# Kernel tuning notes

Measured on AMD Instinct MI355X. Metric: run time of the kernel, lower is better.

Reference implementation:

```python
import jax, jax.numpy as jnp
import numpy as np

DIM = 1024
H = 16
DH = DIM // H
EPS = 1e-5
NEG = -1e38


def _layernorm(x, g, b):
    m = jnp.mean(x, axis=-1, keepdims=True)
    v = jnp.mean((x - m) ** 2, axis=-1, keepdims=True)
    return (x - m) / jnp.sqrt(v + EPS) * g + b


def setup_inputs() -> dict:
    key = jax.random.key(0)
    ks = jax.random.split(key, 12)
    B, Nq, Nk = 4, 1024, 1024
    Q = jax.random.normal(ks[0], (B, Nq, DIM), dtype=jnp.float32)
    K = jax.random.normal(ks[1], (B, Nk, DIM), dtype=jnp.float32)
    V = jax.random.normal(ks[2], (B, Nk, DIM), dtype=jnp.float32)
    mask_Q = jax.random.randint(ks[3], (B, Nq), 0, 2).astype(jnp.bool_)
    mask_K = jax.random.randint(ks[4], (B, Nk), 0, 2).astype(jnp.bool_)
    s = 0.02
    Wq = jax.random.normal(ks[5], (DIM, DIM), dtype=jnp.float32) * s
    Wk = jax.random.normal(ks[6], (DIM, DIM), dtype=jnp.float32) * s
    Wv = jax.random.normal(ks[7], (DIM, DIM), dtype=jnp.float32) * s
    Wo = jax.random.normal(ks[8], (DIM, DIM), dtype=jnp.float32) * s
    ln1_g = jnp.ones((DIM,), jnp.float32); ln1_b = jnp.zeros((DIM,), jnp.float32)
    ln2_g = jnp.ones((DIM,), jnp.float32); ln2_b = jnp.zeros((DIM,), jnp.float32)
    return {"Q": Q, "K": K, "V": V, "Wq": Wq, "Wk": Wk, "Wv": Wv, "Wo": Wo,
            "ln1_g": ln1_g, "ln1_b": ln1_b, "ln2_g": ln2_g, "ln2_b": ln2_b,
            "mask_Q": mask_Q, "mask_K": mask_K}


def reference(Q, K, V, Wq, Wk, Wv, Wo, ln1_g, ln1_b, ln2_g, ln2_b, mask_Q, mask_K):
    B, Nq, _ = Q.shape
    Nk = K.shape[1]
    # zero out padded tokens before projection (mask_tensors)
    Qm = jnp.where(mask_Q[..., None], 0.0, Q)
    Km = jnp.where(mask_K[..., None], 0.0, K)
    Vm = jnp.where(mask_K[..., None], 0.0, V)
    # projections (bias=False); torch Linear stores W as [out, in]
    Qp = Qm @ Wq.T
    Kp = Km @ Wk.T
    Vp = Vm @ Wv.T
    # split heads: [B, N, H, DH]
    Qh = Qp.reshape(B, Nq, H, DH)
    Kh = Kp.reshape(B, Nk, H, DH)
    Vh = Vp.reshape(B, Nk, H, DH)
    # NOTE: original scales by sqrt(dim_V), not sqrt(head_dim)
    scores = jnp.einsum('bqhd,bkhd->bhqk', Qh, Kh) / jnp.sqrt(jnp.float32(DIM))
    pad = mask_Q[:, None, :, None] | mask_K[:, None, None, :]  # [B,1,Nq,Nk]
    A = jax.nn.softmax(jnp.where(pad, NEG, scores), axis=-1)
    A = jnp.where(pad, 0.0, A)  # post-softmax masked_fill (dropout = identity in eval)
    O = jnp.einsum('bhqk,bkhd->bqhd', A, Vh).reshape(B, Nq, DIM)
    mq = mask_Q[..., None]
    # residual uses the PROJECTED Q
    O = Qp + O
    O = jnp.where(mq, 0.0, _layernorm(O, ln1_g, ln1_b))
    # masked fc_o then exact (non-tanh) GELU; gelu(0)=0 so masking commutes
    h = jnp.where(mq, 0.0, O @ Wo.T)
    O = O + jax.nn.gelu(h, approximate=False)
    O = jnp.where(mq, 0.0, _layernorm(O, ln2_g, ln2_b))
    return O
```

## Files before the change

### kernel.cpp

```cpp
#include <hip/hip_runtime.h>

#define NTOK 4096
#define AST 72

typedef _Float16 half4v __attribute__((ext_vector_type(4)));
typedef _Float16 half8 __attribute__((ext_vector_type(8)));
typedef float floatx4 __attribute__((ext_vector_type(4)));

__device__ __forceinline__ half8 cvt8(float4 a, float4 b) {
  half8 h;
  h[0] = (_Float16)a.x; h[1] = (_Float16)a.y; h[2] = (_Float16)a.z; h[3] = (_Float16)a.w;
  h[4] = (_Float16)b.x; h[5] = (_Float16)b.y; h[6] = (_Float16)b.z; h[7] = (_Float16)b.w;
  return h;
}

#if defined(__has_builtin)
#if __has_builtin(__builtin_amdgcn_global_load_lds)
#define HAS_GLL 1
#endif
#endif

#ifdef HAS_GLL
#define STAGE16(gp, lp)                                                        \
  __builtin_amdgcn_global_load_lds(                                           \
      (const __attribute__((address_space(1))) void*)(gp),                     \
      (__attribute__((address_space(3))) void*)(lp), 16, 0, 0)
#else
#define STAGE16(gp, lp)                                                        \
  do { *(half8*)((_Float16*)(lp) + lane * 8) = *(const half8*)(gp); } while (0)
#endif

__device__ __forceinline__ int mask_is_bytes(const int* p) {
  int bad = 0;
#pragma unroll
  for (int i = 0; i < 64; i++) bad |= (((unsigned int)p[i]) > 1u);
  return bad;
}

__global__ __launch_bounds__(256) void cvt_all(
    const float* __restrict__ Q, const float* __restrict__ K, const float* __restrict__ V,
    const float* __restrict__ Wq, const float* __restrict__ Wk, const float* __restrict__ Wv,
    const float* __restrict__ Wo,
    const int* __restrict__ srcQ, const int* __restrict__ srcK,
    _Float16* __restrict__ Xq, _Float16* __restrict__ Xk, _Float16* __restrict__ Xv,
    _Float16* __restrict__ Wqh, _Float16* __restrict__ Wkh, _Float16* __restrict__ Wvh,
    _Float16* __restrict__ Woh,
    int* __restrict__ dstQ, int* __restrict__ dstK)
{
  const int blk = blockIdx.x;
  if (blk >= 8192) {
    const int t = (blk - 8192) * 256 + threadIdx.x;
    const int bq = mask_is_bytes(srcQ);
    const int bk = mask_is_bytes(srcK);
    dstQ[t] = bq ? (int)((const unsigned char*)srcQ)[t] : srcQ[t];
    dstK[t] = bk ? (int)((const unsigned char*)srcK)[t] : srcK[t];
    return;
  }
  const float* src; _Float16* dst; size_t off;
  if      (blk < 2048) { src = Q;  dst = Xq;  off = (size_t)blk * 2048; }
  else if (blk < 4096) { src = K;  dst = Xk;  off = (size_t)(blk - 2048) * 2048; }
  else if (blk < 6144) { src = V;  dst = Xv;  off = (size_t)(blk - 4096) * 2048; }
  else if (blk < 6656) { src = Wq; dst = Wqh; off = (size_t)(blk - 6144) * 2048; }
  else if (blk < 7168) { src = Wk; dst = Wkh; off = (size_t)(blk - 6656) * 2048; }
  else if (blk < 7680) { src = Wv; dst = Wvh; off = (size_t)(blk - 7168) * 2048; }
  else                 { src = Wo; dst = Woh; off = (size_t)(blk - 7680) * 2048; }
  const size_t i = off + (size_t)threadIdx.x * 8;
  const float4 a = *(const float4*)(src + i);
  const float4 b = *(const float4*)(src + i + 4);
  *(half8*)(dst + i) = cvt8(a, b);
}

#define GEMM97_CORE(AH, BH)                                                    \
  __shared__ _Float16 sA[2][128 * 32];                                         \
  __shared__ _Float16 sB[2][128 * 32];                                         \
  const int t = threadIdx.x;                                                   \
  const int bn = blockIdx.y, bm = blockIdx.x;                                  \
  const int lane = t & 63, wv = t >> 6, quad = lane >> 4, l16 = lane & 15;     \
  const int wm = wv & 1, wn = wv >> 1;                                         \
  const int srow = wv * 32 + (lane >> 2);                                      \
  const int scol = (lane & 3) * 8;                                             \
  floatx4 acc[4][4] = {};                                                      \
  const _Float16* gA = AH + (size_t)(bm * 128 + srow) * 1024 + scol;           \
  const _Float16* gB = BH + (size_t)(bn * 128 + srow) * 1024 + scol;           \
  STAGE16(gA,         &sA[0][(wv * 32) * 32]);                                 \
  STAGE16(gA + 16384, &sA[0][(wv * 32 + 16) * 32]);                            \
  STAGE16(gB,         &sB[0][(wv * 32) * 32]);                                 \
  STAGE16(gB + 16384, &sB[0][(wv * 32 + 16) * 32]);                            \
  __syncthreads();                                                             \
  for (int kt = 0; kt < 32; kt++) {                                            \
    const int cur = kt & 1;                                                    \
    if (kt < 31) {                                                             \
      STAGE16(gA + (kt + 1) * 32,         &sA[cur ^ 1][(wv * 32) * 32]);       \
      STAGE16(gA + (kt + 1) * 32 + 16384, &sA[cur ^ 1][(wv * 32 + 16) * 32]);  \
      STAGE16(gB + (kt + 1) * 32,         &sB[cur ^ 1][(wv * 32) * 32]);       \
      STAGE16(gB + (kt + 1) * 32 + 16384, &sB[cur ^ 1][(wv * 32 + 16) * 32]);  \
    }                                                                          \
    half8 af[4], bf[4];                                                        \
    _Pragma("unroll")                                                          \
    for (int s = 0; s < 4; s++)                                                \
      af[s] = *(const half8*)&sA[cur][(wm * 64 + s * 16 + l16) * 32 + quad * 8]; \
    _Pragma("unroll")                                                          \
    for (int u = 0; u < 4; u++)                                                \
      bf[u] = *(const half8*)&sB[cur][(wn * 64 + u * 16 + l16) * 32 + quad * 8]; \
    _Pragma("unroll")                                                          \
    for (int s = 0; s < 4; s++)                                                \
      _Pragma("unroll")                                                        \
      for (int u = 0; u < 4; u++)                                              \
        acc[s][u] = __builtin_amdgcn_mfma_f32_16x16x32_f16(af[s], bf[u],       \
                                                           acc[s][u], 0, 0, 0); \
    __syncthreads();                                                           \
  }

__global__ __launch_bounds__(256) void qkv_gemm(
    const _Float16* __restrict__ Xq, const _Float16* __restrict__ Xk,
    const _Float16* __restrict__ Xv,
    const _Float16* __restrict__ Wqh, const _Float16* __restrict__ Wkh,
    const _Float16* __restrict__ Wvh,
    const int* __restrict__ mQ, const int* __restrict__ mK,
    _Float16* __restrict__ Qh, _Float16* __restrict__ Kh, _Float16* __restrict__ Vh)
{
  const int z = blockIdx.z;
  const _Float16* AH = (z == 0) ? Xq : (z == 1) ? Xk : Xv;
  const _Float16* BH = (z == 0) ? Wqh : (z == 1) ? Wkh : Wvh;
  const int* msk = (z == 0) ? mQ : mK;
  _Float16* out = (z == 0) ? Qh : (z == 1) ? Kh : Vh;
  GEMM97_CORE(AH, BH)
#pragma unroll
  for (int s = 0; s < 4; s++)
#pragma unroll
    for (int rr = 0; rr < 4; rr++) {
      const int row = bm * 128 + wm * 64 + s * 16 + quad * 4 + rr;
      const int m = msk[row];
#pragma unroll
      for (int u = 0; u < 4; u++)
        out[(size_t)row * 1024 + bn * 128 + wn * 64 + u * 16 + l16] =
            m ? (_Float16)0.0f : (_Float16)acc[s][u][rr];
    }
}

__global__ __launch_bounds__(256) void gemm_wo(
    const _Float16* __restrict__ AH, const _Float16* __restrict__ BH,
    const float* __restrict__ X1, float* __restrict__ O2)
{
  __shared__ _Float16 sA[2][128 * 32];
  __shared__ _Float16 sB[2][64 * 32];
  const int t = threadIdx.x;
  const int bn = blockIdx.y, bm = blockIdx.x;
  const int lane = t & 63, wv = t >> 6, quad = lane >> 4, l16 = lane & 15;
  const int srowA = wv * 32 + (lane >> 2);
  const int srowB = wv * 16 + (lane >> 2);
  const int scol = (lane & 3) * 8;
  floatx4 acc[2][4] = {};
  const _Float16* gA = AH + (size_t)(bm * 128 + srowA) * 1024 + scol;
  const _Float16* gB = BH + (size_t)(bn * 64 + srowB) * 1024 + scol;
  STAGE16(gA,         &sA[0][(wv * 32) * 32]);
  STAGE16(gA + 16384, &sA[0][(wv * 32 + 16) * 32]);
  STAGE16(gB,         &sB[0][(wv * 16) * 32]);
  __syncthreads();
  for (int kt = 0; kt < 32; kt++) {
    const int cur = kt & 1;
    if (kt < 31) {
      STAGE16(gA + (kt + 1) * 32,         &sA[cur ^ 1][(wv * 32) * 32]);
      STAGE16(gA + (kt + 1) * 32 + 16384, &sA[cur ^ 1][(wv * 32 + 16) * 32]);
      STAGE16(gB + (kt + 1) * 32,         &sB[cur ^ 1][(wv * 16) * 32]);
    }
    half8 af[2], bf[4];
#pragma unroll
    for (int s = 0; s < 2; s++)
      af[s] = *(const half8*)&sA[cur][(wv * 32 + s * 16 + l16) * 32 + quad * 8];
#pragma unroll
    for (int u = 0; u < 4; u++)
      bf[u] = *(const half8*)&sB[cur][(u * 16 + l16) * 32 + quad * 8];
#pragma unroll
    for (int s = 0; s < 2; s++)
#pragma unroll
      for (int u = 0; u < 4; u++)
        acc[s][u] = __builtin_amdgcn_mfma_f32_16x16x32_f16(af[s], bf[u],
                                                           acc[s][u], 0, 0, 0);
    __syncthreads();
  }
#pragma unroll
  for (int s = 0; s < 2; s++)
#pragma unroll
    for (int rr = 0; rr < 4; rr++) {
      const int row = bm * 128 + wv * 32 + s * 16 + quad * 4 + rr;
#pragma unroll
      for (int u = 0; u < 4; u++) {
        const size_t idx = (size_t)row * 1024 + bn * 64 + u * 16 + l16;
        const float hv = acc[s][u][rr];
        const float ge = 0.5f * hv * (1.0f + erff(hv * 0.70710678118654752f));
        O2[idx] = X1[idx] + ge;
      }
    }
}

__global__ __launch_bounds__(256) void v_transpose(
    const _Float16* __restrict__ Vh, _Float16* __restrict__ Vt)
{
  __shared__ _Float16 sT[64 * AST];
  const int t = threadIdx.x;
  const int kt = blockIdx.x, bh = blockIdx.y;
  const int b = bh >> 4, h = bh & 15;
  const int r = t >> 2, c0 = (t & 3) * 16;
  const _Float16* src = Vh + (size_t)(b * 1024 + kt * 64 + r) * 1024 + h * 64 + c0;
  *(half8*)&sT[r * AST + c0] = *(const half8*)src;
  *(half8*)&sT[r * AST + c0 + 8] = *(const half8*)(src + 8);
  __syncthreads();
  half8 o0, o1;
#pragma unroll
  for (int j = 0; j < 8; j++) o0[j] = sT[(c0 + j) * AST + r];
#pragma unroll
  for (int j = 0; j < 8; j++) o1[j] = sT[(c0 + 8 + j) * AST + r];
  _Float16* dst = Vt + ((size_t)bh * 64 + r) * 1024 + kt * 64 + c0;
  *(half8*)dst = o0;
  *(half8*)(dst + 8) = o1;
}

__global__ __launch_bounds__(256) void attn_mfma3(
    const _Float16* __restrict__ Qh, const _Float16* __restrict__ Kh,
    const _Float16* __restrict__ Vt, const int* __restrict__ maskQ,
    const int* __restrict__ maskK, float* __restrict__ O1)
{
  __shared__ _Float16 sK[64 * AST];
  __shared__ _Float16 sV[64 * AST];
  __shared__ _Float16 sQP[64 * AST];
  __shared__ float bias[1024];

  const int t = threadIdx.x;
  const int qt = blockIdx.x, bh = blockIdx.y;
  const int b = bh >> 4, h = bh & 15;
  const int q0 = qt * 64;
  const size_t base = (size_t)b * 1024;
  const int wv = t >> 6, lane = t & 63, quad = lane >> 4, l16 = lane & 15;
  const int r = t >> 2, c0 = (t & 3) * 16;

  const _Float16* kbase = Kh + (base + r) * 1024 + h * 64 + c0;
  const _Float16* vbase = Vt + ((size_t)bh * 64 + r) * 1024 + c0;
  half8 k0v = *(const half8*)kbase;
  half8 k1v = *(const half8*)(kbase + 8);
  half8 v0v = *(const half8*)vbase;
  half8 v1v = *(const half8*)(vbase + 8);

  for (int i = t; i < 1024; i += 256)
    bias[i] = maskK[b * 1024 + i] ? -1e30f : 0.0f;

  {
    const _Float16* qp = Qh + (base + q0 + r) * 1024 + h * 64 + c0;
    *(half8*)&sQP[r * AST + c0] = *(const half8*)qp;
    *(half8*)&sQP[r * AST + c0 + 8] = *(const half8*)(qp + 8);
  }
  __syncthreads();

  const half8 bq0 = *(const half8*)&sQP[(wv * 16 + l16) * AST + quad * 8];
  const half8 bq1 = *(const half8*)&sQP[(wv * 16 + l16) * AST + 32 + quad * 8];

  float l_i = 0.0f;
  floatx4 acc_o[4] = {};

  for (int kt = 0; kt < 16; kt++) {
    __syncthreads();
    *(half8*)&sK[r * AST + c0]     = k0v;
    *(half8*)&sK[r * AST + c0 + 8] = k1v;
    *(half8*)&sV[r * AST + c0]     = v0v;
    *(half8*)&sV[r * AST + c0 + 8] = v1v;
    __syncthreads();

    if (kt < 15) {
      const _Float16* kp = kbase + (size_t)(kt + 1) * 64 * 1024;
      const _Float16* vp = vbase + (kt + 1) * 64;
      k0v = *(const half8*)kp;
      k1v = *(const half8*)(kp + 8);
      v0v = *(const half8*)vp;
      v1v = *(const half8*)(vp + 8);
    }

    floatx4 s[4] = {};
    __builtin_amdgcn_s_setprio(1);
#pragma unroll
    for (int mt = 0; mt < 4; mt++) {
      const half8 ak0 = *(const half8*)&sK[(mt * 16 + l16) * AST + quad * 8];
      const half8 ak1 = *(const half8*)&sK[(mt * 16 + l16) * AST + 32 + quad * 8];
      s[mt] = __builtin_amdgcn_mfma_f32_16x16x32_f16(ak0, bq0, s[mt], 0, 0, 0);
      s[mt] = __builtin_amdgcn_mfma_f32_16x16x32_f16(ak1, bq1, s[mt], 0, 0, 0);
    }
    __builtin_amdgcn_s_setprio(0);

    float rsum = 0.0f;
#pragma unroll
    for (int mt = 0; mt < 4; mt++) {
      const float4 b4 = *(const float4*)&bias[kt * 64 + mt * 16 + quad * 4];
      const float p0 = __expf(s[mt][0] * 0.03125f + b4.x);
      const float p1 = __expf(s[mt][1] * 0.03125f + b4.y);
      const float p2 = __expf(s[mt][2] * 0.03125f + b4.z);
      const float p3 = __expf(s[mt][3] * 0.03125f + b4.w);
      s[mt][0] = p0; s[mt][1] = p1; s[mt][2] = p2; s[mt][3] = p3;
      rsum += (p0 + p1) + (p2 + p3);
    }
    rsum += __shfl_xor(rsum, 16);
    rsum += __shfl_xor(rsum, 32);
    l_i += rsum;

#pragma unroll
    for (int mt = 0; mt < 4; mt++) {
      half4v pv;
      pv[0] = (_Float16)s[mt][0]; pv[1] = (_Float16)s[mt][1];
      pv[2] = (_Float16)s[mt][2]; pv[3] = (_Float16)s[mt][3];
      *(half4v*)&sQP[(wv * 16 + l16) * AST + mt * 16 + quad * 4] = pv;
    }

    const half8 ap0 = *(const half8*)&sQP[(wv * 16 + l16) * AST + quad * 8];
    const half8 ap1 = *(const half8*)&sQP[(wv * 16 + l16) * AST + 32 + quad * 8];
    __builtin_amdgcn_s_setprio(1);
#pragma unroll
    for (int nt = 0; nt < 4; nt++) {
      const half8 bv0 = *(const half8*)&sV[(nt * 16 + l16) * AST + quad * 8];
      const half8 bv1 = *(const half8*)&sV[(nt * 16 + l16) * AST + 32 + quad * 8];
      acc_o[nt] = __builtin_amdgcn_mfma_f32_16x16x32_f16(ap0, bv0, acc_o[nt], 0, 0, 0);
      acc_o[nt] = __builtin_amdgcn_mfma_f32_16x16x32_f16(ap1, bv1, acc_o[nt], 0, 0, 0);
    }
    __builtin_amdgcn_s_setprio(0);
  }

  float il[4];
#pragma unroll
  for (int rr = 0; rr < 4; rr++) {
    const float lq = __shfl(l_i, quad * 4 + rr);
    il[rr] = (lq > 0.0f) ? 1.0f / lq : 0.0f;
  }
#pragma unroll
  for (int rr = 0; rr < 4; rr++) {
    const int row = q0 + wv * 16 + quad * 4 + rr;
    const int mq = maskQ[b * 1024 + row];
#pragma unroll
    for (int nt = 0; nt < 4; nt++) {
      const size_t gi = (base + row) * 1024 + h * 64 + nt * 16 + l16;
      O1[gi] = mq ? 0.0f : ((float)Qh[gi] + acc_o[nt][rr] * il[rr]);
    }
  }
}

__device__ __forceinline__ void ln_stats(float4 x, int t, float* mean, float* rinv) {
  float s = x.x + x.y + x.z + x.w;
  float s2 = x.x * x.x + x.y * x.y + x.z * x.z + x.w * x.w;
#pragma unroll
  for (int off = 32; off >= 1; off >>= 1) { s += __shfl_xor(s, off); s2 += __shfl_xor(s2, off); }
  __shared__ float red[8];
  __shared__ float sm[2];
  const int wv = t >> 6, lane = t & 63;
  if (lane == 0) { red[wv] = s; red[4 + wv] = s2; }
  __syncthreads();
  if (t == 0) {
    const float S = red[0] + red[1] + red[2] + red[3];
    const float S2 = red[4] + red[5] + red[6] + red[7];
    const float m = S * (1.0f / 1024.0f);
    const float v = S2 * (1.0f / 1024.0f) - m * m;
    sm[0] = m; sm[1] = rsqrtf(v + 1e-5f);
  }
  __syncthreads();
  *mean = sm[0]; *rinv = sm[1];
}

__global__ __launch_bounds__(256) void ln_f32(
    const float* __restrict__ X, const float* __restrict__ g,
    const float* __restrict__ bta, const int* __restrict__ mask,
    float* __restrict__ out)
{
  const int rr = blockIdx.x, t = threadIdx.x, c = 4 * t;
  const float4 x = *(const float4*)&X[(size_t)rr * 1024 + c];
  float mean, ri;
  ln_stats(x, t, &mean, &ri);
  const int msk = mask[rr];
  const float4 gg = *(const float4*)&g[c];
  const float4 bb = *(const float4*)&bta[c];
  float4 o;
  o.x = msk ? 0.f : (x.x - mean) * ri * gg.x + bb.x;
  o.y = msk ? 0.f : (x.y - mean) * ri * gg.y + bb.y;
  o.z = msk ? 0.f : (x.z - mean) * ri * gg.z + bb.z;
  o.w = msk ? 0.f : (x.w - mean) * ri * gg.w + bb.w;
  *(float4*)&out[(size_t)rr * 1024 + c] = o;
}

__global__ __launch_bounds__(256) void ln_f32h(
    const float* __restrict__ X, const float* __restrict__ g,
    const float* __restrict__ bta, const int* __restrict__ mask,
    float* __restrict__ out, _Float16* __restrict__ outh)
{
  const int rr = blockIdx.x, t = threadIdx.x, c = 4 * t;
  const float4 x = *(const float4*)&X[(size_t)rr * 1024 + c];
  float mean, ri;
  ln_stats(x, t, &mean, &ri);
  const int msk = mask[rr];
  const float4 gg = *(const float4*)&g[c];
  const float4 bb = *(const float4*)&bta[c];
  float4 o;
  o.x = msk ? 0.f : (x.x - mean) * ri * gg.x + bb.x;
  o.y = msk ? 0.f : (x.y - mean) * ri * gg.y + bb.y;
  o.z = msk ? 0.f : (x.z - mean) * ri * gg.z + bb.z;
  o.w = msk ? 0.f : (x.w - mean) * ri * gg.w + bb.w;
  const size_t idx = (size_t)rr * 1024 + c;
  *(float4*)&out[idx] = o;
  half4v hh;
  hh[0] = (_Float16)o.x; hh[1] = (_Float16)o.y;
  hh[2] = (_Float16)o.z; hh[3] = (_Float16)o.w;
  *(half4v*)&outh[idx] = hh;
}

extern "C" void kernel_launch(void* const* d_in, const int* in_sizes, int n_in,
                              void* d_out, int out_size, void* d_ws, size_t ws_size,
                              hipStream_t stream)
{
  const float* Q  = (const float*)d_in[0];
  const float* K  = (const float*)d_in[1];
  const float* V  = (const float*)d_in[2];
  const float* Wq = (const float*)d_in[3];
  const float* Wk = (const float*)d_in[4];
  const float* Wv = (const float*)d_in[5];
  const float* Wo = (const float*)d_in[6];
  const float* g1 = (const float*)d_in[7];
  const float* b1 = (const float*)d_in[8];
  const float* g2 = (const float*)d_in[9];
  const float* b2 = (const float*)d_in[10];
  float* out = (float*)d_out;

  char* base = (char*)d_ws;
  const size_t MB_ = 1024 * 1024;
  _Float16* Xq  = (_Float16*)(base +  0 * MB_);
  _Float16* Xk  = (_Float16*)(base +  8 * MB_);
  _Float16* Xv  = (_Float16*)(base + 16 * MB_);
  _Float16* Wqh = (_Float16*)(base + 24 * MB_);
  _Float16* Wkh = (_Float16*)(base + 26 * MB_);
  _Float16* Wvh = (_Float16*)(base + 28 * MB_);
  _Float16* Woh = (_Float16*)(base + 30 * MB_);
  _Float16* Qh  = (_Float16*)(base + 32 * MB_);
  _Float16* Kh  = (_Float16*)(base + 40 * MB_);
  _Float16* Vh  = (_Float16*)(base + 48 * MB_);
  _Float16* Vt  = (_Float16*)(base + 56 * MB_);
  float*    O1  = (float*)(base + 64 * MB_);
  int*      mQ  = (int*)(base + 80 * MB_);
  int*      mK  = mQ + NTOK;
  float*    X1  = (float*)(base + 0 * MB_);
  _Float16* X1h = (_Float16*)(base + 16 * MB_);
  float*    O2  = (float*)(base + 32 * MB_);

  const dim3 bb(256);
  cvt_all<<<dim3(8208), bb, 0, stream>>>(Q, K, V, Wq, Wk, Wv, Wo,
                                         (const int*)d_in[11], (const int*)d_in[12],
                                         Xq, Xk, Xv, Wqh, Wkh, Wvh, Woh, mQ, mK);
  qkv_gemm<<<dim3(32, 8, 3), bb, 0, stream>>>(Xq, Xk, Xv, Wqh, Wkh, Wvh,
                                              mQ, mK, Qh, Kh, Vh);
  v_transpose<<<dim3(16, 64), bb, 0, stream>>>(Vh, Vt);
  attn_mfma3<<<dim3(16, 64), bb, 0, stream>>>(Qh, Kh, Vt, mQ, mK, O1);
  ln_f32h<<<dim3(4096), bb, 0, stream>>>(O1, g1, b1, mQ, X1, X1h);
  gemm_wo<<<dim3(32, 16), bb, 0, stream>>>(X1h, Woh, X1, O2);
  ln_f32<<<dim3(4096), bb, 0, stream>>>(O2, g2, b2, mQ, out);
}
```

Measured before the change: 249.9 us.

## Fuse V transpose into QKV GEMM epilogue and reuse 128x128 core for Wo GEMM

```diff
diff --git a/kernel.cpp b/kernel.cpp
--- a/kernel.cpp
+++ b/kernel.cpp
@@ -117,103 +117,76 @@
     const _Float16* __restrict__ Wqh, const _Float16* __restrict__ Wkh,
     const _Float16* __restrict__ Wvh,
     const int* __restrict__ mQ, const int* __restrict__ mK,
-    _Float16* __restrict__ Qh, _Float16* __restrict__ Kh, _Float16* __restrict__ Vh)
+    _Float16* __restrict__ Qh, _Float16* __restrict__ Kh, _Float16* __restrict__ Vt)
 {
   const int z = blockIdx.z;
   const _Float16* AH = (z == 0) ? Xq : (z == 1) ? Xk : Xv;
   const _Float16* BH = (z == 0) ? Wqh : (z == 1) ? Wkh : Wvh;
-  const int* msk = (z == 0) ? mQ : mK;
-  _Float16* out = (z == 0) ? Qh : (z == 1) ? Kh : Vh;
   GEMM97_CORE(AH, BH)
-#pragma unroll
-  for (int s = 0; s < 4; s++)
-#pragma unroll
-    for (int rr = 0; rr < 4; rr++) {
-      const int row = bm * 128 + wm * 64 + s * 16 + quad * 4 + rr;
-      const int m = msk[row];
-#pragma unroll
-      for (int u = 0; u < 4; u++)
-        out[(size_t)row * 1024 + bn * 128 + wn * 64 + u * 16 + l16] =
-            m ? (_Float16)0.0f : (_Float16)acc[s][u][rr];
-    }
+  if (z < 2) {
+    const int* msk = (z == 0) ? mQ : mK;
+    _Float16* out = (z == 0) ? Qh : Kh;
+#pragma unroll
+    for (int s = 0; s < 4; s++)
+#pragma unroll
+      for (int rr = 0; rr < 4; rr++) {
+        const int row = bm * 128 + wm * 64 + s * 16 + quad * 4 + rr;
+        const int m = msk[row];
+#pragma unroll
+        for (int u = 0; u < 4; u++)
+          out[(size_t)row * 1024 + bn * 128 + wn * 64 + u * 16 + l16] =
+              m ? (_Float16)0.0f : (_Float16)acc[s][u][rr];
+      }
+  } else {
+    _Float16* scr = (wv == 0) ? &sA[0][0] : (wv == 1) ? &sA[1][0]
+                  : (wv == 2) ? &sB[0][0] : &sB[1][0];
+    const int h = 2 * bn + wn;
+    const int krow0 = bm * 128 + wm * 64;
+    const int bq = krow0 >> 10;
+    const int kloc = krow0 & 1023;
+    const int dl = lane & 31, kh = lane >> 5;
+#pragma unroll
+    for (int p = 0; p < 2; p++) {
+#pragma unroll
+      for (int up = 0; up < 2; up++) {
+        const int u = p * 2 + up;
+#pragma unroll
+        for (int s = 0; s < 4; s++)
+#pragma unroll
+          for (int rr = 0; rr < 4; rr++)
+            scr[(s * 16 + quad * 4 + rr) * 36 + up * 16 + l16] =
+                (_Float16)acc[s][u][rr];
+      }
+      half8 o[4];
+#pragma unroll
+      for (int j = 0; j < 32; j++)
+        ((_Float16*)o)[j] = scr[(kh * 32 + j) * 36 + dl];
+      _Float16* dst = Vt + ((size_t)((bq * 16 + h) * 64 + p * 32 + dl)) * 1024
+                         + kloc + kh * 32;
+      *(half8*)dst = o[0]; *(half8*)(dst + 8) = o[1];
+      *(half8*)(dst + 16) = o[2]; *(half8*)(dst + 24) = o[3];
+    }
+  }
 }
 
 __global__ __launch_bounds__(256) void gemm_wo(
     const _Float16* __restrict__ AH, const _Float16* __restrict__ BH,
     const float* __restrict__ X1, float* __restrict__ O2)
 {
-  __shared__ _Float16 sA[2][128 * 32];
-  __shared__ _Float16 sB[2][64 * 32];
-  const int t = threadIdx.x;
-  const int bn = blockIdx.y, bm = blockIdx.x;
-  const int lane = t & 63, wv = t >> 6, quad = lane >> 4, l16 = lane & 15;
-  const int srowA = wv * 32 + (lane >> 2);
-  const int srowB = wv * 16 + (lane >> 2);
-  const int scol = (lane & 3) * 8;
-  floatx4 acc[2][4] = {};
-  const _Float16* gA = AH + (size_t)(bm * 128 + srowA) * 1024 + scol;
-  const _Float16* gB = BH + (size_t)(bn * 64 + srowB) * 1024 + scol;
-  STAGE16(gA,         &sA[0][(wv * 32) * 32]);
-  STAGE16(gA + 16384, &sA[0][(wv * 32 + 16) * 32]);
-  STAGE16(gB,         &sB[0][(wv * 16) * 32]);
-  __syncthreads();
-  for (int kt = 0; kt < 32; kt++) {
-    const int cur = kt & 1;
-    if (kt < 31) {
-      STAGE16(gA + (kt + 1) * 32,         &sA[cur ^ 1][(wv * 32) * 32]);
-      STAGE16(gA + (kt + 1) * 32 + 16384, &sA[cur ^ 1][(wv * 32 + 16) * 32]);
-      STAGE16(gB + (kt + 1) * 32,         &sB[cur ^ 1][(wv * 16) * 32]);
-    }
-    half8 af[2], bf[4];
-#pragma unroll
-    for (int s = 0; s < 2; s++)
-      af[s] = *(const half8*)&sA[cur][(wv * 32 + s * 16 + l16) * 32 + quad * 8];
-#pragma unroll
-    for (int u = 0; u < 4; u++)
-      bf[u] = *(const half8*)&sB[cur][(u * 16 + l16) * 32 + quad * 8];
-#pragma unroll
-    for (int s = 0; s < 2; s++)
-#pragma unroll
-      for (int u = 0; u < 4; u++)
-        acc[s][u] = __builtin_amdgcn_mfma_f32_16x16x32_f16(af[s], bf[u],
-                                                           acc[s][u], 0, 0, 0);
-    __syncthreads();
-  }
-#pragma unroll
-  for (int s = 0; s < 2; s++)
+  GEMM97_CORE(AH, BH)
+#pragma unroll
+  for (int s = 0; s < 4; s++)
 #pragma unroll
     for (int rr = 0; rr < 4; rr++) {
-      const int row = bm * 128 + wv * 32 + s * 16 + quad * 4 + rr;
+      const int row = bm * 128 + wm * 64 + s * 16 + quad * 4 + rr;
 #pragma unroll
       for (int u = 0; u < 4; u++) {
-        const size_t idx = (size_t)row * 1024 + bn * 64 + u * 16 + l16;
+        const size_t idx = (size_t)row * 1024 + bn * 128 + wn * 64 + u * 16 + l16;
         const float hv = acc[s][u][rr];
         const float ge = 0.5f * hv * (1.0f + erff(hv * 0.70710678118654752f));
         O2[idx] = X1[idx] + ge;
       }
     }
-}
-
-__global__ __launch_bounds__(256) void v_transpose(
-    const _Float16* __restrict__ Vh, _Float16* __restrict__ Vt)
-{
-  __shared__ _Float16 sT[64 * AST];
-  const int t = threadIdx.x;
-  const int kt = blockIdx.x, bh = blockIdx.y;
-  const int b = bh >> 4, h = bh & 15;
-  const int r = t >> 2, c0 = (t & 3) * 16;
-  const _Float16* src = Vh + (size_t)(b * 1024 + kt * 64 + r) * 1024 + h * 64 + c0;
-  *(half8*)&sT[r * AST + c0] = *(const half8*)src;
-  *(half8*)&sT[r * AST + c0 + 8] = *(const half8*)(src + 8);
-  __syncthreads();
-  half8 o0, o1;
-#pragma unroll
-  for (int j = 0; j < 8; j++) o0[j] = sT[(c0 + j) * AST + r];
-#pragma unroll
-  for (int j = 0; j < 8; j++) o1[j] = sT[(c0 + 8 + j) * AST + r];
-  _Float16* dst = Vt + ((size_t)bh * 64 + r) * 1024 + kt * 64 + c0;
-  *(half8*)dst = o0;
-  *(half8*)(dst + 8) = o1;
 }
 
 __global__ __launch_bounds__(256) void attn_mfma3(
@@ -433,7 +406,6 @@
   _Float16* Woh = (_Float16*)(base + 30 * MB_);
   _Float16* Qh  = (_Float16*)(base + 32 * MB_);
   _Float16* Kh  = (_Float16*)(base + 40 * MB_);
-  _Float16* Vh  = (_Float16*)(base + 48 * MB_);
   _Float16* Vt  = (_Float16*)(base + 56 * MB_);
   float*    O1  = (float*)(base + 64 * MB_);
   int*      mQ  = (int*)(base + 80 * MB_);
@@ -447,10 +419,9 @@
                                          (const int*)d_in[11], (const int*)d_in[12],
                                          Xq, Xk, Xv, Wqh, Wkh, Wvh, Woh, mQ, mK);
   qkv_gemm<<<dim3(32, 8, 3), bb, 0, stream>>>(Xq, Xk, Xv, Wqh, Wkh, Wvh,
-                                              mQ, mK, Qh, Kh, Vh);
-  v_transpose<<<dim3(16, 64), bb, 0, stream>>>(Vh, Vt);
+                                              mQ, mK, Qh, Kh, Vt);
   attn_mfma3<<<dim3(16, 64), bb, 0, stream>>>(Qh, Kh, Vt, mQ, mK, O1);
   ln_f32h<<<dim3(4096), bb, 0, stream>>>(O1, g1, b1, mQ, X1, X1h);
-  gemm_wo<<<dim3(32, 16), bb, 0, stream>>>(X1h, Woh, X1, O2);
+  gemm_wo<<<dim3(32, 8), bb, 0, stream>>>(X1h, Woh, X1, O2);
   ln_f32<<<dim3(4096), bb, 0, stream>>>(O2, g2, b2, mQ, out);
 }
```

After: 274.8 us. 1.1x slower.
